# Optimization experiments

Hardware: AMD Instinct MI355X
Metric: run time of the kernel (lower is better)

## Reference

```python
import jax, jax.numpy as jnp
import numpy as np

B, D, H, NL, NB = 131072, 64, 512, 3, 8
d = D // 2
EPS = 1e-5


def _mlp(x, W0, b0, Wh, bh, Wo, bo, act):
    # x: [B, d] -> [B, d]; hidden width H, NL hidden->hidden layers, linear output
    h = act(x @ W0 + b0)
    for i in range(Wh.shape[0]):
        h = act(h @ Wh[i] + bh[i])
    return h @ Wo + bo


def setup_inputs() -> dict:
    key = jax.random.key(0)
    ks = jax.random.split(key, 16)
    s = 0.05
    inp = {
        "y": jax.random.normal(ks[0], (B, D), dtype=jnp.float32),
        # s-network params, stacked over blocks
        "sW0": jax.random.normal(ks[1], (NB, d, H), dtype=jnp.float32) * s,
        "sb0": jnp.zeros((NB, H), jnp.float32),
        "sWh": jax.random.normal(ks[2], (NB, NL, H, H), dtype=jnp.float32) * s,
        "sbh": jnp.zeros((NB, NL, H), jnp.float32),
        "sWo": jax.random.normal(ks[3], (NB, H, d), dtype=jnp.float32) * s,
        "sbo": jnp.zeros((NB, d), jnp.float32),
        # t-network params
        "tW0": jax.random.normal(ks[4], (NB, d, H), dtype=jnp.float32) * s,
        "tb0": jnp.zeros((NB, H), jnp.float32),
        "tWh": jax.random.normal(ks[5], (NB, NL, H, H), dtype=jnp.float32) * s,
        "tbh": jnp.zeros((NB, NL, H), jnp.float32),
        "tWo": jax.random.normal(ks[6], (NB, H, d), dtype=jnp.float32) * s,
        "tbo": jnp.zeros((NB, d), jnp.float32),
        # BatchNorm flow params (log_gamma, beta init at 0 as in torch module)
        "bn_log_gamma": jnp.zeros((NB, D), jnp.float32),
        "bn_beta": jnp.zeros((NB, D), jnp.float32),
    }
    return inp


def reference(y, sW0, sb0, sWh, sbh, sWo, sbo,
              tW0, tb0, tWh, tbh, tWo, tbo,
              bn_log_gamma, bn_beta):
    act_s, act_t = jnp.tanh, jax.nn.relu
    log_det = jnp.zeros((y.shape[0], 1), y.dtype)
    for b in range(NB):
        # alternating slice/compliment: even blocks condition on first half
        if b % 2 == 0:
            ys, yc = y[:, :d], y[:, d:]
        else:
            ys, yc = y[:, d:], y[:, :d]
        s_out = _mlp(ys, sW0[b], sb0[b], sWh[b], sbh[b], sWo[b], sbo[b], act_s)
        t_out = _mlp(ys, tW0[b], tb0[b], tWh[b], tbh[b], tWo[b], tbo[b], act_t)
        zc = yc * jnp.exp(s_out) + t_out
        z = jnp.concatenate([ys, zc], axis=1) if b % 2 == 0 else jnp.concatenate([zc, ys], axis=1)
        log_det = log_det + jnp.sum(s_out, axis=1, keepdims=True)
        # Batch_Norm flow (training mode: batch stats, unbiased var like torch .var(0))
        mean = z.mean(axis=0)
        var = z.var(axis=0, ddof=1)
        x_hat = (z - mean) / jnp.sqrt(var + EPS)
        y = jnp.exp(bn_log_gamma[b]) * x_hat + bn_beta[b]
        log_det = log_det + jnp.sum(bn_log_gamma[b] - 0.5 * jnp.log(var + EPS))
    return y, log_det
```

## Files before the change

### kernel.cpp

```cpp
#include <hip/hip_runtime.h>

#define NBLK 8
#define BROWS 131072
#define HDIM 512
#define EPSV 1e-5f
#define WROWS 64

typedef __bf16 bf16x8 __attribute__((ext_vector_type(8)));
typedef __bf16 bf16x4 __attribute__((ext_vector_type(4)));
typedef float f32x4 __attribute__((ext_vector_type(4)));

#define PACK_NET 819200
#define PACK_H 16384
#define PACK_HEAD 802816

__device__ __forceinline__ float act_tanh_f(float x) {
  float e = __expf(x + x);
  return fmaf(-2.f, __builtin_amdgcn_rcpf(e + 1.f), 1.f);
}

template <int ACT>
__device__ __forceinline__ float apply_act(float v) {
  if (ACT == 1) return act_tanh_f(v);
  return fmaxf(v, 0.f);
}

template <int ACT, int PHASE, bool CHAIN>
__device__ __forceinline__ void dense_hidden(const __bf16* __restrict__ Wp,
                                             const __bf16* __restrict__ Wn,
                                             const float* __restrict__ bias,
                                             __bf16* hb, bf16x8 (&br)[3][4],
                                             int w, int c, int quad, int lane) {
  f32x4 acc[4][4];
#pragma unroll
  for (int rb = 0; rb < 4; ++rb)
#pragma unroll
    for (int ft = 0; ft < 4; ++ft) acc[rb][ft] = (f32x4){0.f, 0.f, 0.f, 0.f};
  const __bf16* wp = Wp + (size_t)(w * 2) * 16384 + lane * 8;
  const __bf16* wn = Wn + (size_t)(w * 2) * 16384 + lane * 8;
  const int msk = (c & 7) << 3;
  __builtin_amdgcn_s_setprio(1);
#pragma unroll
  for (int kt = 0; kt < 16; ++kt) {
    const int pf = kt + 2;
    if (pf < 16) {
#pragma unroll
      for (int ft = 0; ft < 4; ++ft)
        br[(pf + PHASE) % 3][ft] = *(const bf16x8*)(wp + (ft >> 1) * 16384 +
                                                    (ft & 1) * 512 + pf * 1024);
    } else if (CHAIN) {
#pragma unroll
      for (int ft = 0; ft < 4; ++ft)
        br[(pf + PHASE) % 3][ft] = *(const bf16x8*)(wn + (ft >> 1) * 16384 +
                                                    (ft & 1) * 512 + (pf - 16) * 1024);
    }
    const int sk = (kt * 32 + quad * 8) ^ msk;
#pragma unroll
    for (int rb = 0; rb < 4; ++rb) {
      bf16x8 hv = *(const bf16x8*)&hb[(rb * 16 + c) * HDIM + sk];
#pragma unroll
      for (int ft = 0; ft < 4; ++ft)
        acc[rb][ft] = __builtin_amdgcn_mfma_f32_16x16x32_bf16(br[(kt + PHASE) % 3][ft], hv, acc[rb][ft], 0, 0, 0);
    }
  }
  __builtin_amdgcn_s_setprio(0);
  __syncthreads();
#pragma unroll
  for (int ft = 0; ft < 4; ++ft) {
    const f32x4 bi = *(const f32x4*)&bias[w * 64 + ft * 16 + quad * 4];
    const int fsw = (w * 64 + ft * 16 + quad * 4) ^ msk;
#pragma unroll
    for (int rb = 0; rb < 4; ++rb) {
      bf16x4 pk;
#pragma unroll
      for (int i = 0; i < 4; ++i)
        pk[i] = (__bf16)apply_act<ACT>(acc[rb][ft][i] + bi[i]);
      *(bf16x4*)&hb[(rb * 16 + c) * HDIM + fsw] = pk;
    }
  }
  __syncthreads();
}

template <int ACT>
__device__ __forceinline__ void dense_l0(const __bf16* __restrict__ pw,
                                         const float* __restrict__ b0,
                                         const __bf16* __restrict__ ys,
                                         __bf16* hb, int w, int c, int quad,
                                         int lane) {
  bf16x8 aw[4];
#pragma unroll
  for (int ft = 0; ft < 4; ++ft)
    aw[ft] = *(const bf16x8*)&pw[(size_t)(w * 2 + (ft >> 1)) * 1024 +
                                 (ft & 1) * 512 + lane * 8];
  f32x4 acc[4][4];
#pragma unroll
  for (int rb = 0; rb < 4; ++rb)
#pragma unroll
    for (int ft = 0; ft < 4; ++ft) acc[rb][ft] = (f32x4){0.f, 0.f, 0.f, 0.f};
  const int ysk = (quad * 8) ^ ((c & 3) << 3);
  __builtin_amdgcn_s_setprio(1);
#pragma unroll
  for (int rb = 0; rb < 4; ++rb) {
    bf16x8 yb = *(const bf16x8*)&ys[(rb * 16 + c) * 32 + ysk];
#pragma unroll
    for (int ft = 0; ft < 4; ++ft)
      acc[rb][ft] = __builtin_amdgcn_mfma_f32_16x16x32_bf16(aw[ft], yb, acc[rb][ft], 0, 0, 0);
  }
  __builtin_amdgcn_s_setprio(0);
  const int msk = (c & 7) << 3;
  const int rowb = c << 9;
  const int wq = w * 64 + quad * 4;
#pragma unroll
  for (int ft = 0; ft < 4; ++ft) {
    const f32x4 bi = *(const f32x4*)&b0[wq + ft * 16];
    const int fsw = ((wq + ft * 16) ^ msk) + rowb;
#pragma unroll
    for (int rb = 0; rb < 4; ++rb) {
      bf16x4 pk;
#pragma unroll
      for (int i = 0; i < 4; ++i)
        pk[i] = (__bf16)apply_act<ACT>(acc[rb][ft][i] + bi[i]);
      *(bf16x4*)&hb[fsw + rb * 8192] = pk;
    }
  }
}

__device__ __forceinline__ f32x4 dense_head(const __bf16* __restrict__ ph,
                                            const float* __restrict__ bo,
                                            const __bf16* __restrict__ hb,
                                            int fb, int rb, int c, int quad,
                                            int lane) {
  const __bf16* wp = ph + (size_t)fb * 8192 + lane * 8;
  bf16x8 hr[3];
  hr[0] = *(const bf16x8*)wp;
  hr[1] = *(const bf16x8*)(wp + 512);
  f32x4 acc = (f32x4){0.f, 0.f, 0.f, 0.f};
  const int msk = (c & 7) << 3;
  __builtin_amdgcn_s_setprio(1);
#pragma unroll
  for (int kt = 0; kt < 16; ++kt) {
    if (kt + 2 < 16) hr[(kt + 2) % 3] = *(const bf16x8*)(wp + (kt + 2) * 512);
    bf16x8 hv = *(const bf16x8*)&hb[(rb * 16 + c) * HDIM + ((kt * 32 + quad * 8) ^ msk)];
    acc = __builtin_amdgcn_mfma_f32_16x16x32_bf16(hr[kt % 3], hv, acc, 0, 0, 0);
  }
  __builtin_amdgcn_s_setprio(0);
  const int f0 = fb * 16 + quad * 4;
  f32x4 bo4 = *(const f32x4*)&bo[f0];
#pragma unroll
  for (int i = 0; i < 4; ++i) acc[i] += bo4[i];
  return acc;
}

template <int ACT>
__device__ __forceinline__ f32x4 run_net(const __bf16* __restrict__ pw,
                                         const float* __restrict__ b0,
                                         const float* __restrict__ bh,
                                         const float* __restrict__ bo,
                                         const __bf16* __restrict__ ysb,
                                         __bf16* hbuf, int w, int fb, int rb,
                                         int c, int quad, int lane) {
  const __bf16* W1 = pw + PACK_H;
  const __bf16* W2 = pw + PACK_H + 262144;
  const __bf16* W3 = pw + PACK_H + 2 * 262144;
  dense_l0<ACT>(pw, b0, ysb, hbuf, w, c, quad, lane);
  bf16x8 br[3][4];
  {
    const __bf16* wp1 = W1 + (size_t)(w * 2) * 16384 + lane * 8;
#pragma unroll
    for (int s = 0; s < 2; ++s)
#pragma unroll
      for (int ft = 0; ft < 4; ++ft)
        br[s][ft] = *(const bf16x8*)(wp1 + (ft >> 1) * 16384 + (ft & 1) * 512 +
                                     s * 1024);
  }
  __syncthreads();
  dense_hidden<ACT, 0, true>(W1, W2, bh, hbuf, br, w, c, quad, lane);
  dense_hidden<ACT, 1, true>(W2, W3, bh + 512, hbuf, br, w, c, quad, lane);
  dense_hidden<ACT, 2, false>(W3, W3, bh + 1024, hbuf, br, w, c, quad, lane);
  return dense_head(pw + PACK_HEAD, bo, hbuf, fb, rb, c, quad, lane);
}

template <bool FIRST>
__global__ __launch_bounds__(512, 4) void fused_block(
    const float* __restrict__ src, const __bf16* __restrict__ pwS,
    const __bf16* __restrict__ pwT, const float* __restrict__ sb0,
    const float* __restrict__ sbh, const float* __restrict__ sbo,
    const float* __restrict__ tb0, const float* __restrict__ tbh,
    const float* __restrict__ tbo, const float* __restrict__ prevP,
    float* __restrict__ zbuf, float* __restrict__ ld,
    float* __restrict__ stats_out, int o) {
  __shared__ __bf16 hbuf[WROWS * HDIM];
  __shared__ __bf16 ysb[WROWS * 32];
  const int tid = threadIdx.x;
  const int w = tid >> 6, lane = tid & 63, c = lane & 15, quad = lane >> 4;
  const size_t row0 = (size_t)blockIdx.x * WROWS;

  {
    const int row = tid >> 3, sub = tid & 7;
    const int col0 = o + sub * 4;
    f32x4 yv = *(const f32x4*)&src[(row0 + row) * 64 + col0];
    bf16x4 pv;
#pragma unroll
    for (int j = 0; j < 4; ++j) {
      const float A_ = FIRST ? 1.f : prevP[col0 + j];
      const float C_ = FIRST ? 0.f : prevP[64 + col0 + j];
      pv[j] = (__bf16)fmaf(A_, yv[j], C_);
    }
    *(bf16x4*)&ysb[row * 32 + ((sub * 4) ^ ((row & 3) << 3))] = pv;
  }
  __syncthreads();

  const int fb = w & 1, rb = w >> 1;
  const int f0 = fb * 16 + quad * 4;
  const int r = rb * 16 + c;

  f32x4 tv = run_net<2>(pwT, tb0, tbh, tbo, ysb, hbuf, w, fb, rb, c, quad, lane);
  __syncthreads();

  f32x4 sacc = run_net<1>(pwS, sb0, sbh, sbo, ysb, hbuf, w, fb, rb, c, quad, lane);
  float sv[4];
#pragma unroll
  for (int i = 0; i < 4; ++i) sv[i] = sacc[i];

  const size_t grow = row0 + r;
  __syncthreads();
  float* cs = (float*)hbuf;
  float* lda = cs + 128;
  if (tid < 128) cs[tid] = 0.f;
  else if (tid < 192) lda[tid - 128] = 0.f;
  __syncthreads();

  const int oc = o ^ 32;
  float zc[4], yn2[4];
  {
    f32x4 pA1, pC1, pA2, pC2;
    if (FIRST) {
      pA1 = pA2 = (f32x4){1.f, 1.f, 1.f, 1.f};
      pC1 = pC2 = (f32x4){0.f, 0.f, 0.f, 0.f};
    } else {
      pA1 = *(const f32x4*)&prevP[oc + f0];
      pC1 = *(const f32x4*)&prevP[64 + oc + f0];
      pA2 = *(const f32x4*)&prevP[o + f0];
      pC2 = *(const f32x4*)&prevP[64 + o + f0];
    }
    f32x4 yv = *(const f32x4*)&src[grow * 64 + oc + f0];
    f32x4 zo;
#pragma unroll
    for (int i = 0; i < 4; ++i) {
      zc[i] = fmaf(fmaf(pA1[i], yv[i], pC1[i]), __expf(sv[i]), tv[i]);
      zo[i] = zc[i];
    }
    *(f32x4*)&zbuf[grow * 64 + oc + f0] = zo;
    f32x4 yv2 = *(const f32x4*)&src[grow * 64 + o + f0];
    f32x4 yo;
#pragma unroll
    for (int i = 0; i < 4; ++i) {
      yn2[i] = fmaf(pA2[i], yv2[i], pC2[i]);
      yo[i] = yn2[i];
    }
    *(f32x4*)&zbuf[grow * 64 + o + f0] = yo;
  }

  {
    float ssum = sv[0] + sv[1] + sv[2] + sv[3];
    ssum += __shfl_xor(ssum, 16);
    ssum += __shfl_xor(ssum, 32);
    if (quad == 0) atomicAdd(&lda[r], ssum);
  }

#pragma unroll
  for (int i = 0; i < 4; ++i) {
    float v = zc[i], q = zc[i] * zc[i];
    float v2 = yn2[i], q2 = yn2[i] * yn2[i];
#pragma unroll
    for (int m = 1; m < 16; m <<= 1) {
      v += __shfl_xor(v, m);  q += __shfl_xor(q, m);
      v2 += __shfl_xor(v2, m); q2 += __shfl_xor(q2, m);
    }
    if (c == 0) {
      atomicAdd(&cs[oc + f0 + i], v);
      atomicAdd(&cs[64 + oc + f0 + i], q);
      atomicAdd(&cs[o + f0 + i], v2);
      atomicAdd(&cs[64 + o + f0 + i], q2);
    }
  }
  __syncthreads();
  if (tid < 128) {
    atomicAdd(&stats_out[tid], cs[tid]);
  } else if (tid < 192) {
    const int rr = tid - 128;
    const size_t gr = row0 + rr;
    if (FIRST) ld[gr] = lda[rr]; else ld[gr] += lda[rr];
  }
}


__global__ void stats_kernel(const float* __restrict__ raw,
                             const float* __restrict__ lg,
                             const float* __restrict__ beta,
                             float* __restrict__ param,
                             float* __restrict__ ld_scalar) {
  const int t = threadIdx.x;
  const float S = raw[t], SS = raw[64 + t];
  const float mean = S / (float)BROWS;
  const float var = (SS - S * mean) / (float)(BROWS - 1);
  const float inv = rsqrtf(var + EPSV);
  const float g = __expf(lg[t]);
  const float A = g * inv;
  param[t] = A;
  param[64 + t] = beta[t] - mean * A;
  float contrib = lg[t] - 0.5f * __logf(var + EPSV);
  contrib += __shfl_xor(contrib, 1);  contrib += __shfl_xor(contrib, 2);
  contrib += __shfl_xor(contrib, 4);  contrib += __shfl_xor(contrib, 8);
  contrib += __shfl_xor(contrib, 16); contrib += __shfl_xor(contrib, 32);
  if (t == 0) atomicAdd(ld_scalar, contrib);
}

__global__ void final_kernel(float* __restrict__ out,
                             const float* __restrict__ param7,
                             const float* __restrict__ ld_scalar) {
  const size_t gid = (size_t)blockIdx.x * 256 + threadIdx.x;
  const size_t total = (size_t)BROWS * 64;
  const int col = gid & 63;
  const float z = out[gid];
  out[gid] = param7[col] * z + param7[64 + col];
  if (gid < BROWS) out[total + gid] += ld_scalar[0];
}

__global__ void pack_weights(const float* __restrict__ sW0,
                             const float* __restrict__ sWh,
                             const float* __restrict__ sWo,
                             const float* __restrict__ tW0,
                             const float* __restrict__ tWh,
                             const float* __restrict__ tWo,
                             __bf16* __restrict__ dst) {
  const int gid = blockIdx.x * 256 + threadIdx.x;
  const int gpn = PACK_NET / 8;
  const int b = gid / (2 * gpn);
  const int rr0 = gid % (2 * gpn);
  const int net = rr0 / gpn;
  const size_t o = (size_t)(rr0 % gpn) * 8;
  const float* W0 = net ? tW0 : sW0;
  const float* Wh = net ? tWh : sWh;
  const float* Wo = net ? tWo : sWo;
  __bf16* d = dst + ((size_t)b * 2 + net) * PACK_NET + o;
  float v[8];
  if (o < PACK_H) {
    const int idx = (int)(o >> 3);
    const int lane = idx & 63, fbb = (idx >> 6) & 1, w = (idx >> 7) & 15;
    const int cc = lane & 15, q = lane >> 4;
    const int f = w * 32 + fbb * 16 + cc;
    const float* s = W0 + (size_t)b * 32 * 512;
#pragma unroll
    for (int j = 0; j < 8; ++j) v[j] = s[(size_t)(q * 8 + j) * 512 + f];
  } else if (o < PACK_HEAD) {
    const size_t oo = o - PACK_H;
    const int l = (int)(oo >> 18);
    const int idx = (int)((oo & 262143) >> 3);
    const int lane = idx & 63, fbb = (idx >> 6) & 1, kt = (idx >> 7) & 15,
              w = (idx >> 11) & 15;
    const int cc = lane & 15, q = lane >> 4;
    const int f = w * 32 + fbb * 16 + cc;
    const float* s = Wh + ((size_t)(b * 3 + l)) * 512 * 512;
#pragma unroll
    for (int j = 0; j < 8; ++j) v[j] = s[(size_t)(kt * 32 + q * 8 + j) * 512 + f];
  } else {
    const size_t oo = o - PACK_HEAD;
    const int idx = (int)(oo >> 3);
    const int lane = idx & 63, kt = (idx >> 6) & 15, fbb = (idx >> 10) & 1;
    const int cc = lane & 15, q = lane >> 4;
    const int f = fbb * 16 + cc;
    const float* s = Wo + (size_t)b * 512 * 32;
#pragma unroll
    for (int j = 0; j < 8; ++j) v[j] = s[(size_t)(kt * 32 + q * 8 + j) * 32 + f];
  }
  bf16x8 pv;
#pragma unroll
  for (int j = 0; j < 8; ++j) pv[j] = (__bf16)v[j];
  *(bf16x8*)d = pv;
}


extern "C" void kernel_launch(void* const* d_in, const int* in_sizes, int n_in,
                              void* d_out, int out_size, void* d_ws, size_t ws_size,
                              hipStream_t stream) {
  const float* y_in = (const float*)d_in[0];
  const float* sW0 = (const float*)d_in[1];
  const float* sb0 = (const float*)d_in[2];
  const float* sWh = (const float*)d_in[3];
  const float* sbh = (const float*)d_in[4];
  const float* sWo = (const float*)d_in[5];
  const float* sbo = (const float*)d_in[6];
  const float* tW0 = (const float*)d_in[7];
  const float* tb0 = (const float*)d_in[8];
  const float* tWh = (const float*)d_in[9];
  const float* tbh = (const float*)d_in[10];
  const float* tWo = (const float*)d_in[11];
  const float* tbo = (const float*)d_in[12];
  const float* bn_lg = (const float*)d_in[13];
  const float* bn_bt = (const float*)d_in[14];

  char* p = (char*)d_ws;
  __bf16* packed = (__bf16*)p; p += (size_t)NBLK * 2 * PACK_NET * 2;
  float* stats_raw = (float*)p; p += NBLK * 128 * 4;
  float* ld_scalar = (float*)p; p += 256;
  float* stats_param = (float*)p; p += NBLK * 128 * 4;

  float* out = (float*)d_out;
  float* zbuf = out;
  float* ld = out + (size_t)BROWS * 64;

  pack_weights<<<(NBLK * 2 * PACK_NET / 8) / 256, 256, 0, stream>>>(
      sW0, sWh, sWo, tW0, tWh, tWo, packed);
  hipMemsetAsync(stats_raw, 0, NBLK * 128 * 4 + 256, stream);

  const int GG = BROWS / WROWS;

  for (int b = 0; b < NBLK; ++b) {
    const int o = (b & 1) ? 32 : 0;
    const __bf16* pwS = packed + (size_t)b * 2 * PACK_NET;
    const __bf16* pwT = pwS + PACK_NET;
    float* praw = stats_raw + b * 128;
    const float* srcb = (b == 0) ? y_in : zbuf;

    if (b == 0) {
      fused_block<true><<<GG, 512, 0, stream>>>(srcb, pwS, pwT,
          sb0, sbh, sbo, tb0, tbh, tbo, nullptr, zbuf, ld, praw, o);
    } else {
      fused_block<false><<<GG, 512, 0, stream>>>(srcb, pwS, pwT,
          sb0 + b * 512, sbh + (size_t)b * 1536, sbo + b * 32,
          tb0 + b * 512, tbh + (size_t)b * 1536, tbo + b * 32,
          stats_param + (size_t)(b - 1) * 128, zbuf, ld, praw, o);
    }
    stats_kernel<<<1, 64, 0, stream>>>(praw, bn_lg + b * 64, bn_bt + b * 64,
                                       stats_param + (size_t)b * 128, ld_scalar);
  }

  final_kernel<<<(BROWS * 64) / 256, 256, 0, stream>>>(
      out, stats_param + 7 * 128, ld_scalar);
}
```

Baseline: 3.985 ms.

## Fold batch-norm stats finalization into fused block kernel, drop per-block stats launches

```diff
diff --git a/kernel.cpp b/kernel.cpp
--- a/kernel.cpp
+++ b/kernel.cpp
@@ -25,34 +25,33 @@
   return fmaxf(v, 0.f);
 }
 
-template <int ACT, int PHASE, bool CHAIN>
+template <int ACT>
 __device__ __forceinline__ void dense_hidden(const __bf16* __restrict__ Wp,
-                                             const __bf16* __restrict__ Wn,
                                              const float* __restrict__ bias,
-                                             __bf16* hb, bf16x8 (&br)[3][4],
-                                             int w, int c, int quad, int lane) {
+                                             __bf16* hb, int w, int c,
+                                             int quad, int lane) {
   f32x4 acc[4][4];
 #pragma unroll
   for (int rb = 0; rb < 4; ++rb)
 #pragma unroll
     for (int ft = 0; ft < 4; ++ft) acc[rb][ft] = (f32x4){0.f, 0.f, 0.f, 0.f};
   const __bf16* wp = Wp + (size_t)(w * 2) * 16384 + lane * 8;
-  const __bf16* wn = Wn + (size_t)(w * 2) * 16384 + lane * 8;
+  bf16x8 br[3][4];
+#pragma unroll
+  for (int s = 0; s < 2; ++s)
+#pragma unroll
+    for (int ft = 0; ft < 4; ++ft)
+      br[s][ft] = *(const bf16x8*)(wp + (ft >> 1) * 16384 + (ft & 1) * 512 +
+                                   s * 1024);
   const int msk = (c & 7) << 3;
   __builtin_amdgcn_s_setprio(1);
 #pragma unroll
   for (int kt = 0; kt < 16; ++kt) {
-    const int pf = kt + 2;
-    if (pf < 16) {
+    if (kt + 2 < 16) {
 #pragma unroll
       for (int ft = 0; ft < 4; ++ft)
-        br[(pf + PHASE) % 3][ft] = *(const bf16x8*)(wp + (ft >> 1) * 16384 +
-                                                    (ft & 1) * 512 + pf * 1024);
-    } else if (CHAIN) {
-#pragma unroll
-      for (int ft = 0; ft < 4; ++ft)
-        br[(pf + PHASE) % 3][ft] = *(const bf16x8*)(wn + (ft >> 1) * 16384 +
-                                                    (ft & 1) * 512 + (pf - 16) * 1024);
+        br[(kt + 2) % 3][ft] = *(const bf16x8*)(wp + (ft >> 1) * 16384 +
+                                                (ft & 1) * 512 + (kt + 2) * 1024);
     }
     const int sk = (kt * 32 + quad * 8) ^ msk;
 #pragma unroll
@@ -60,7 +59,7 @@
       bf16x8 hv = *(const bf16x8*)&hb[(rb * 16 + c) * HDIM + sk];
 #pragma unroll
       for (int ft = 0; ft < 4; ++ft)
-        acc[rb][ft] = __builtin_amdgcn_mfma_f32_16x16x32_bf16(br[(kt + PHASE) % 3][ft], hv, acc[rb][ft], 0, 0, 0);
+        acc[rb][ft] = __builtin_amdgcn_mfma_f32_16x16x32_bf16(br[kt % 3][ft], hv, acc[rb][ft], 0, 0, 0);
     }
   }
   __builtin_amdgcn_s_setprio(0);
@@ -159,24 +158,11 @@
                                          const __bf16* __restrict__ ysb,
                                          __bf16* hbuf, int w, int fb, int rb,
                                          int c, int quad, int lane) {
-  const __bf16* W1 = pw + PACK_H;
-  const __bf16* W2 = pw + PACK_H + 262144;
-  const __bf16* W3 = pw + PACK_H + 2 * 262144;
   dense_l0<ACT>(pw, b0, ysb, hbuf, w, c, quad, lane);
-  bf16x8 br[3][4];
-  {
-    const __bf16* wp1 = W1 + (size_t)(w * 2) * 16384 + lane * 8;
-#pragma unroll
-    for (int s = 0; s < 2; ++s)
-#pragma unroll
-      for (int ft = 0; ft < 4; ++ft)
-        br[s][ft] = *(const bf16x8*)(wp1 + (ft >> 1) * 16384 + (ft & 1) * 512 +
-                                     s * 1024);
-  }
-  __syncthreads();
-  dense_hidden<ACT, 0, true>(W1, W2, bh, hbuf, br, w, c, quad, lane);
-  dense_hidden<ACT, 1, true>(W2, W3, bh + 512, hbuf, br, w, c, quad, lane);
-  dense_hidden<ACT, 2, false>(W3, W3, bh + 1024, hbuf, br, w, c, quad, lane);
+  __syncthreads();
+  dense_hidden<ACT>(pw + PACK_H, bh, hbuf, w, c, quad, lane);
+  dense_hidden<ACT>(pw + PACK_H + 262144, bh + 512, hbuf, w, c, quad, lane);
+  dense_hidden<ACT>(pw + PACK_H + 2 * 262144, bh + 1024, hbuf, w, c, quad, lane);
   return dense_head(pw + PACK_HEAD, bo, hbuf, fb, rb, c, quad, lane);
 }
 
@@ -186,14 +172,34 @@
     const __bf16* __restrict__ pwT, const float* __restrict__ sb0,
     const float* __restrict__ sbh, const float* __restrict__ sbo,
     const float* __restrict__ tb0, const float* __restrict__ tbh,
-    const float* __restrict__ tbo, const float* __restrict__ prevP,
+    const float* __restrict__ tbo, const float* __restrict__ prevR,
+    const float* __restrict__ lgm, const float* __restrict__ btm,
     float* __restrict__ zbuf, float* __restrict__ ld,
     float* __restrict__ stats_out, int o) {
   __shared__ __bf16 hbuf[WROWS * HDIM];
   __shared__ __bf16 ysb[WROWS * 32];
+  __shared__ __align__(16) float pl[132];
   const int tid = threadIdx.x;
   const int w = tid >> 6, lane = tid & 63, c = lane & 15, quad = lane >> 4;
   const size_t row0 = (size_t)blockIdx.x * WROWS;
+
+  if (!FIRST) {
+    const int t = lane;
+    const float S = prevR[t], SS = prevR[64 + t];
+    const float mean = S / (float)BROWS;
+    const float var = (SS - S * mean) / (float)(BROWS - 1);
+    const float inv = rsqrtf(var + EPSV);
+    const float g = __expf(lgm[t]);
+    const float A = g * inv;
+    pl[t] = A;
+    pl[64 + t] = btm[t] - mean * A;
+    float contrib = lgm[t] - 0.5f * __logf(var + EPSV);
+    contrib += __shfl_xor(contrib, 1);  contrib += __shfl_xor(contrib, 2);
+    contrib += __shfl_xor(contrib, 4);  contrib += __shfl_xor(contrib, 8);
+    contrib += __shfl_xor(contrib, 16); contrib += __shfl_xor(contrib, 32);
+    if (t == 0) pl[128] = contrib;
+    __syncthreads();
+  }
 
   {
     const int row = tid >> 3, sub = tid & 7;
@@ -202,8 +208,8 @@
     bf16x4 pv;
 #pragma unroll
     for (int j = 0; j < 4; ++j) {
-      const float A_ = FIRST ? 1.f : prevP[col0 + j];
-      const float C_ = FIRST ? 0.f : prevP[64 + col0 + j];
+      const float A_ = FIRST ? 1.f : pl[col0 + j];
+      const float C_ = FIRST ? 0.f : pl[64 + col0 + j];
       pv[j] = (__bf16)fmaf(A_, yv[j], C_);
     }
     *(bf16x4*)&ysb[row * 32 + ((sub * 4) ^ ((row & 3) << 3))] = pv;
@@ -238,10 +244,10 @@
       pA1 = pA2 = (f32x4){1.f, 1.f, 1.f, 1.f};
       pC1 = pC2 = (f32x4){0.f, 0.f, 0.f, 0.f};
     } else {
-      pA1 = *(const f32x4*)&prevP[oc + f0];
-      pC1 = *(const f32x4*)&prevP[64 + oc + f0];
-      pA2 = *(const f32x4*)&prevP[o + f0];
-      pC2 = *(const f32x4*)&prevP[64 + o + f0];
+      pA1 = *(const f32x4*)&pl[oc + f0];
+      pC1 = *(const f32x4*)&pl[64 + oc + f0];
+      pA2 = *(const f32x4*)&pl[o + f0];
+      pC2 = *(const f32x4*)&pl[64 + o + f0];
     }
     f32x4 yv = *(const f32x4*)&src[grow * 64 + oc + f0];
     f32x4 zo;
@@ -290,7 +296,8 @@
   } else if (tid < 192) {
     const int rr = tid - 128;
     const size_t gr = row0 + rr;
-    if (FIRST) ld[gr] = lda[rr]; else ld[gr] += lda[rr];
+    if (FIRST) ld[gr] = lda[rr];
+    else ld[gr] += lda[rr] + pl[128];
   }
 }
 
@@ -425,17 +432,19 @@
 
     if (b == 0) {
       fused_block<true><<<GG, 512, 0, stream>>>(srcb, pwS, pwT,
-          sb0, sbh, sbo, tb0, tbh, tbo, nullptr, zbuf, ld, praw, o);
+          sb0, sbh, sbo, tb0, tbh, tbo, nullptr, nullptr, nullptr,
+          zbuf, ld, praw, o);
     } else {
       fused_block<false><<<GG, 512, 0, stream>>>(srcb, pwS, pwT,
           sb0 + b * 512, sbh + (size_t)b * 1536, sbo + b * 32,
           tb0 + b * 512, tbh + (size_t)b * 1536, tbo + b * 32,
-          stats_param + (size_t)(b - 1) * 128, zbuf, ld, praw, o);
-    }
-    stats_kernel<<<1, 64, 0, stream>>>(praw, bn_lg + b * 64, bn_bt + b * 64,
-                                       stats_param + (size_t)b * 128, ld_scalar);
-  }
-
+          stats_raw + (size_t)(b - 1) * 128, bn_lg + (b - 1) * 64,
+          bn_bt + (b - 1) * 64, zbuf, ld, praw, o);
+    }
+  }
+  stats_kernel<<<1, 64, 0, stream>>>(stats_raw + 7 * 128, bn_lg + 7 * 64,
+                                     bn_bt + 7 * 64, stats_param + 7 * 128,
+                                     ld_scalar);
   final_kernel<<<(BROWS * 64) / 256, 256, 0, stream>>>(
       out, stats_param + 7 * 128, ld_scalar);
 }
```

Measured after the change: 3.968 ms (median of 2 runs). About the same (-0.4%).
